# Performance work log

Measured on AMD Instinct MI355X. Metric: run time of the kernel, lower is better.

The kernel has to match this reference:

```python
import jax, jax.numpy as jnp
import numpy as np

N = 100000      # num vertices
NE = 20000      # num hyperedges
NNZ = 1600000   # incidence pairs
NFEAT = 128
NHID = 64       # nhid * nhead = 8 * 8
NCLASS = 40
NLAYER = 4
ALPHA = 0.1
LAMDA = 0.5


def setup_inputs() -> dict:
    key = jax.random.key(0)
    ks = jax.random.split(key, 9)
    x = jax.random.normal(ks[0], (N, NFEAT), dtype=jnp.float32)
    vertex = jax.random.randint(ks[1], (NNZ,), 0, N, dtype=jnp.int32)
    edges = jax.random.randint(ks[2], (NNZ,), 0, NE, dtype=jnp.int32)
    degE = jax.random.uniform(ks[3], (NE, 1), dtype=jnp.float32)
    degV = jax.random.uniform(ks[4], (N, 1), dtype=jnp.float32)
    W0 = jax.random.normal(ks[5], (NFEAT, NHID), dtype=jnp.float32) * 0.05
    b0 = jnp.zeros((NHID,), jnp.float32)
    Ws = jax.random.normal(ks[6], (NLAYER, NHID, NHID), dtype=jnp.float32) * 0.05
    Wout = jax.random.normal(ks[7], (NHID, NCLASS), dtype=jnp.float32) * 0.05
    bout = jnp.zeros((NCLASS,), jnp.float32)
    return dict(x=x, degE=degE, degV=degV, W0=W0, b0=b0, Ws=Ws,
                Wout=Wout, bout=bout, vertex=vertex, edges=edges)


def _normalize_l2(X):
    # torch: norm computed on detached X, inf scales zeroed
    norm = jnp.linalg.norm(jax.lax.stop_gradient(X), axis=1, keepdims=True)
    scale = jnp.where(norm > 0, 1.0 / norm, 0.0)
    return X * scale


def reference(x, degE, degV, W0, b0, Ws, Wout, bout, vertex, edges):
    # per-hyperedge member counts for the 'mean' first_aggregate
    counts = jax.ops.segment_sum(jnp.ones((NNZ,), x.dtype), edges, num_segments=NE)
    counts = jnp.maximum(counts, 1.0)[:, None]  # [NE,1]

    X = jax.nn.relu(x @ W0 + b0)   # [N, NHID]
    X0 = X
    for i in range(NLAYER):
        beta = float(np.log(LAMDA / (i + 1) + 1.0))
        Xve = X[vertex]                                                   # [NNZ, NHID]
        Xe = jax.ops.segment_sum(Xve, edges, num_segments=NE) / counts   # vertex->edge mean
        Xe = Xe * degE                                                    # [NE, NHID]
        Xev = Xe[edges]                                                   # [NNZ, NHID]
        Xv = jax.ops.segment_sum(Xev, vertex, num_segments=N) * degV     # edge->vertex sum
        Xn = _normalize_l2(Xv)                                            # use_norm=True
        Xi = (1.0 - ALPHA) * Xn + ALPHA * X0
        X = jax.nn.relu((1.0 - beta) * Xi + beta * (Xi @ Ws[i]))
    logits = X @ Wout + bout
    return jax.nn.log_softmax(logits, axis=1)
```

## Files before the change

kernel.cpp:

```cpp
#include <hip/hip_runtime.h>
#include <math.h>

constexpr int NV   = 100000;
constexpr int NEg  = 20000;
constexpr int NNZp = 1600000;
constexpr int NF   = 128;
constexpr int NH   = 64;
constexpr int NC   = 40;

constexpr int WE  = 64;
constexpr int NBE = (NEg + WE - 1) / WE;
constexpr int WV  = 256;
constexpr int NBV = (NV + WV - 1) / WV;
constexpr int CAPS = 6400;
constexpr int CH   = 4096;
constexpr int PBLK = (NNZp + CH - 1) / CH;

typedef __bf16 bf16x8 __attribute__((ext_vector_type(8)));
typedef float  f32x4  __attribute__((ext_vector_type(4)));
typedef unsigned short u16x8 __attribute__((ext_vector_type(8)));

__device__ __forceinline__ float bf2f(unsigned short u) {
    unsigned int x = ((unsigned int)u) << 16;
    return __builtin_bit_cast(float, x);
}
__device__ __forceinline__ unsigned short f2bf(float f) {
    unsigned int x = __builtin_bit_cast(unsigned int, f);
    x += 0x7fffu + ((x >> 16) & 1u);
    return (unsigned short)(x >> 16);
}
__device__ __forceinline__ ushort4 pack4(float a, float b, float c, float d) {
    ushort4 u; u.x = f2bf(a); u.y = f2bf(b); u.z = f2bf(c); u.w = f2bf(d);
    return u;
}

__device__ __forceinline__ int block_excl_scan(int val, int tid, int* wtot) {
    __syncthreads();
    int x = val;
#pragma unroll
    for (int o = 1; o < 64; o <<= 1) {
        int y = __shfl_up(x, o);
        if ((tid & 63) >= o) x += y;
    }
    if ((tid & 63) == 63) wtot[tid >> 6] = x;
    __syncthreads();
    int add = 0;
    const int w = tid >> 6;
#pragma unroll
    for (int k = 0; k < 7; ++k) add += (k < w) ? wtot[k] : 0;
    return add + x - val;
}

__global__ __launch_bounds__(256) void coarse_hist(const int* __restrict__ vertex,
                                                   const int* __restrict__ edges,
                                                   int* __restrict__ cnt_be,
                                                   int* __restrict__ cnt_bv) {
    __shared__ int he[NBE], hv[NBV];
    for (int i = threadIdx.x; i < NBE; i += 256) he[i] = 0;
    for (int i = threadIdx.x; i < NBV; i += 256) hv[i] = 0;
    __syncthreads();
    const int base = blockIdx.x * CH;
    const int end  = min(base + CH, NNZp);
    for (int i = base + threadIdx.x; i < end; i += 256) {
        atomicAdd(&he[edges[i]  >> 6], 1);
        atomicAdd(&hv[vertex[i] >> 8], 1);
    }
    __syncthreads();
    for (int i = threadIdx.x; i < NBE; i += 256) if (he[i]) atomicAdd(&cnt_be[i], he[i]);
    for (int i = threadIdx.x; i < NBV; i += 256) if (hv[i]) atomicAdd(&cnt_bv[i], hv[i]);
}

__global__ __launch_bounds__(512) void scan_buckets(const int* __restrict__ cnt_be,
                                                    const int* __restrict__ cnt_bv,
                                                    int* __restrict__ rsb_e,
                                                    int* __restrict__ rsb_v,
                                                    int* __restrict__ rs_e,
                                                    int* __restrict__ rs_v) {
    __shared__ int s[512];
    const int n      = (blockIdx.x == 0) ? NBE : NBV;
    const int* c     = (blockIdx.x == 0) ? cnt_be : cnt_bv;
    int* r           = (blockIdx.x == 0) ? rsb_e : rsb_v;
    const int t = threadIdx.x;
    int v = (t < n) ? c[t] : 0;
    s[t] = v;
    __syncthreads();
    for (int o = 1; o < 512; o <<= 1) {
        int u = (t >= o) ? s[t - o] : 0;
        __syncthreads();
        s[t] += u;
        __syncthreads();
    }
    if (t < n) r[t] = s[t] - v;
    if (t == 0) {
        r[n] = NNZp;
        if (blockIdx.x == 0) rs_e[NEg] = NNZp;
        else                 rs_v[NV]  = NNZp;
    }
}

__global__ __launch_bounds__(512) void partition_both(const int* __restrict__ vertex,
                                                      const int* __restrict__ edges,
                                                      const int* __restrict__ rsb_e,
                                                      const int* __restrict__ rsb_v,
                                                      int* __restrict__ gcur_e,
                                                      int* __restrict__ gcur_v,
                                                      int* __restrict__ vid_out,
                                                      int* __restrict__ eid_out) {
    __shared__ int sval_e[CH], sdst_e[CH];
    __shared__ int sval_v[CH], sdst_v[CH];
    __shared__ int hist_e[NBE], off_e[NBE], gbase_e[NBE], cnt_e[NBE];
    __shared__ int hist_v[NBV], off_v[NBV], gbase_v[NBV], cnt_v[NBV];
    __shared__ int wtot[8];
    const int tid = threadIdx.x;
    for (int i = tid; i < NBE; i += 512) { hist_e[i] = 0; cnt_e[i] = 0; }
    for (int i = tid; i < NBV; i += 512) { hist_v[i] = 0; cnt_v[i] = 0; }
    __syncthreads();
    const int base = blockIdx.x * CH;
    const int n    = min(base + CH, NNZp) - base;
    for (int i = tid; i < n; i += 512) {
        atomicAdd(&hist_e[edges[base + i]  >> 6], 1);
        atomicAdd(&hist_v[vertex[base + i] >> 8], 1);
    }
    __syncthreads();
    {
        int hv_ = (tid < NBE) ? hist_e[tid] : 0;
        int ex  = block_excl_scan(hv_, tid, wtot);
        if (tid < NBE) {
            off_e[tid]   = ex;
            gbase_e[tid] = rsb_e[tid] + (hv_ ? atomicAdd(&gcur_e[tid], hv_) : 0);
        }
    }
    {
        int hv_ = (tid < NBV) ? hist_v[tid] : 0;
        int ex  = block_excl_scan(hv_, tid, wtot);
        if (tid < NBV) {
            off_v[tid]   = ex;
            gbase_v[tid] = rsb_v[tid] + (hv_ ? atomicAdd(&gcur_v[tid], hv_) : 0);
        }
    }
    __syncthreads();
    for (int i = tid; i < n; i += 512) {
        int e = edges[base + i];
        int v = vertex[base + i];
        int fe = e >> 6;
        int rk = atomicAdd(&cnt_e[fe], 1);
        int sl = off_e[fe] + rk;
        sval_e[sl] = (v << 6) | (e & 63);
        sdst_e[sl] = gbase_e[fe] + rk;
        int fv = v >> 8;
        int rv = atomicAdd(&cnt_v[fv], 1);
        int s2 = off_v[fv] + rv;
        sval_v[s2] = (e << 8) | (v & 255);
        sdst_v[s2] = gbase_v[fv] + rv;
    }
    __syncthreads();
    for (int i = tid; i < n; i += 512) {
        vid_out[sdst_e[i]] = sval_e[i];
        eid_out[sdst_v[i]] = sval_v[i];
    }
}

__global__ __launch_bounds__(512) void local_sort_both(const int* __restrict__ rsb_e,
                                                       const int* __restrict__ rsb_v,
                                                       int* __restrict__ vid_buf,
                                                       int* __restrict__ eid_buf,
                                                       int* __restrict__ rs_e,
                                                       int* __restrict__ rs_v,
                                                       const float* __restrict__ degE,
                                                       float* __restrict__ scaleE) {
    __shared__ int stage[CAPS];
    __shared__ int hist[256], off[256], cnt2[256];
    const bool eside = blockIdx.x < NBE;
    const int b   = eside ? blockIdx.x : blockIdx.x - NBE;
    const int W   = eside ? 64 : 256;
    const int FB  = eside ? 6 : 8;
    const int NID = eside ? NEg : NV;
    const int* rsb = eside ? rsb_e : rsb_v;
    int* buf       = eside ? vid_buf : eid_buf;
    int* rs        = eside ? rs_e : rs_v;
    const int base = rsb[b];
    const int sz   = rsb[b + 1] - base;
    const int tid = threadIdx.x;
    if (tid < 256) { hist[tid] = 0; cnt2[tid] = 0; }
    __syncthreads();
    for (int t = tid; t < sz; t += 512) atomicAdd(&hist[buf[base + t] & (W - 1)], 1);
    __syncthreads();
    {
        int v = (tid < W) ? hist[tid] : 0;
        if (tid < W) off[tid] = v;
        __syncthreads();
        for (int o = 1; o < W; o <<= 1) {
            int u = (tid < W && tid >= o) ? off[tid - o] : 0;
            __syncthreads();
            if (tid < W) off[tid] += u;
            __syncthreads();
        }
        if (tid < W) off[tid] -= v;
    }
    if (tid < W) {
        int gid = b * W + tid;
        if (gid < NID) {
            rs[gid] = base + off[tid];
            if (eside) {
                int c = hist[tid];
                scaleE[gid] = degE[gid] / (float)(c < 1 ? 1 : c);
            }
        }
    }
    __syncthreads();
    for (int t = tid; t < sz; t += 512) {
        int w = buf[base + t];
        int f = w & (W - 1);
        int rk = off[f] + atomicAdd(&cnt2[f], 1);
        stage[rk] = w >> FB;
    }
    __syncthreads();
    for (int t = tid; t < sz; t += 512) buf[base + t] = stage[t];
}

__global__ __launch_bounds__(256) void make_wfrag(const float* __restrict__ Ws,
                                                  const float* __restrict__ Wout,
                                                  const float* __restrict__ W0,
                                                  unsigned short* __restrict__ frag) {
    int t = blockIdx.x * 256 + threadIdx.x;
    int lane = t & 63;
    int g = t >> 6;
    int quad = lane >> 4, cl = lane & 15;
    unsigned short o[8];
    if (g < 32) {
        int li = g >> 3, w = (g >> 1) & 3, kh = g & 1;
        int n = w * 16 + cl;
#pragma unroll
        for (int j = 0; j < 8; ++j) {
            int k = kh * 32 + quad * 8 + j;
            o[j] = f2bf(Ws[(size_t)li * NH * NH + k * NH + n]);
        }
    } else if (g < 40) {
        int w = (g - 32) >> 1, kh = g & 1;
        int n = w * 16 + cl;
#pragma unroll
        for (int j = 0; j < 8; ++j) {
            int k = kh * 32 + quad * 8 + j;
            o[j] = (n < NC) ? f2bf(Wout[k * NC + n]) : (unsigned short)0;
        }
    } else {
        int w = (g - 40) >> 2, kb = (g - 40) & 3;
        int n = w * 16 + cl;
#pragma unroll
        for (int j = 0; j < 8; ++j) {
            int k = kb * 32 + quad * 8 + j;
            o[j] = f2bf(W0[k * NH + n]);
        }
    }
    unsigned short* dst = frag + (size_t)g * 512 + lane * 8;
    *((ushort4*)dst)       = *(ushort4*)&o[0];
    *((ushort4*)(dst + 4)) = *(ushort4*)&o[4];
}

__global__ __launch_bounds__(256) void gemm0_kernel(const float* __restrict__ x,
                                                    const unsigned short* __restrict__ W0frag,
                                                    const float* __restrict__ b0,
                                                    unsigned short* __restrict__ Xbf,
                                                    unsigned short* __restrict__ X0bf) {
    __shared__ unsigned short xs[16][136];
    const int tid = threadIdx.x;
    const int r  = tid >> 4;
    const int c8 = (tid & 15) * 8;
    const int rowbase = blockIdx.x * 16;
    float4 p0 = *((const float4*)(x + (size_t)(rowbase + r) * NF + c8));
    float4 p1 = *((const float4*)(x + (size_t)(rowbase + r) * NF + c8 + 4));
    *((ushort4*)&xs[r][c8])     = pack4(p0.x, p0.y, p0.z, p0.w);
    *((ushort4*)&xs[r][c8 + 4]) = pack4(p1.x, p1.y, p1.z, p1.w);
    __syncthreads();
    const int lane = tid & 63;
    const int wv   = tid >> 6;
    const int quad = lane >> 4;
    const int cl   = lane & 15;
    f32x4 acc = {0.f, 0.f, 0.f, 0.f};
#pragma unroll
    for (int kb = 0; kb < 4; ++kb) {
        bf16x8 a = *((const bf16x8*)&xs[cl][kb * 32 + quad * 8]);
        bf16x8 b = *((const bf16x8*)(W0frag + ((size_t)(wv * 4 + kb) * 64 + lane) * 8));
        acc = __builtin_amdgcn_mfma_f32_16x16x32_bf16(a, b, acc, 0, 0, 0);
    }
    const int col = wv * 16 + cl;
    const float bo = b0[col];
#pragma unroll
    for (int p = 0; p < 4; ++p) {
        const int orow = quad * 4 + p;
        float o = acc[p] + bo;
        o = o > 0.f ? o : 0.f;
        unsigned short ob = f2bf(o);
        const size_t idx = (size_t)(rowbase + orow) * NH + col;
        Xbf[idx]  = ob;
        X0bf[idx] = ob;
    }
}

__global__ __launch_bounds__(256) void gather_ve(const int* __restrict__ rs_e,
                                                 const int* __restrict__ vid_sorted,
                                                 const unsigned short* __restrict__ Xbf,
                                                 const float* __restrict__ scaleE,
                                                 unsigned short* __restrict__ Xebf) {
    const int tid = threadIdx.x;
    const int l8  = tid & 7;
    const int e = blockIdx.x * 16 + (tid >> 4);
    const int sb = rs_e[e];
    const int se = rs_e[e + 1];
    const int h  = (se - sb + 1) >> 1;
    int m        = sb + ((tid & 8) ? h : 0);
    const int en = (tid & 8) ? se : (sb + h);
    float a[8] = {0.f, 0.f, 0.f, 0.f, 0.f, 0.f, 0.f, 0.f};
    if (m + 4 <= en) {
        int i0 = vid_sorted[m], i1 = vid_sorted[m + 1];
        int i2 = vid_sorted[m + 2], i3 = vid_sorted[m + 3];
        m += 4;
        while (m + 4 <= en) {
            int j0 = vid_sorted[m], j1 = vid_sorted[m + 1];
            int j2 = vid_sorted[m + 2], j3 = vid_sorted[m + 3];
            m += 4;
            u16x8 p = *((const u16x8*)(Xbf + (size_t)i0 * NH) + l8);
            u16x8 q = *((const u16x8*)(Xbf + (size_t)i1 * NH) + l8);
            u16x8 u = *((const u16x8*)(Xbf + (size_t)i2 * NH) + l8);
            u16x8 t = *((const u16x8*)(Xbf + (size_t)i3 * NH) + l8);
#pragma unroll
            for (int j = 0; j < 8; ++j)
                a[j] += bf2f(p[j]) + bf2f(q[j]) + bf2f(u[j]) + bf2f(t[j]);
            i0 = j0; i1 = j1; i2 = j2; i3 = j3;
        }
        u16x8 p = *((const u16x8*)(Xbf + (size_t)i0 * NH) + l8);
        u16x8 q = *((const u16x8*)(Xbf + (size_t)i1 * NH) + l8);
        u16x8 u = *((const u16x8*)(Xbf + (size_t)i2 * NH) + l8);
        u16x8 t = *((const u16x8*)(Xbf + (size_t)i3 * NH) + l8);
#pragma unroll
        for (int j = 0; j < 8; ++j)
            a[j] += bf2f(p[j]) + bf2f(q[j]) + bf2f(u[j]) + bf2f(t[j]);
    }
    for (; m < en; ++m) {
        u16x8 p = *((const u16x8*)(Xbf + (size_t)vid_sorted[m] * NH) + l8);
#pragma unroll
        for (int j = 0; j < 8; ++j) a[j] += bf2f(p[j]);
    }
#pragma unroll
    for (int j = 0; j < 8; ++j) a[j] += __shfl_xor(a[j], 8);
    if (!(tid & 8)) {
        const float s = scaleE[e];
        u16x8 o;
#pragma unroll
        for (int j = 0; j < 8; ++j) o[j] = f2bf(a[j] * s);
        *((u16x8*)(Xebf + (size_t)e * NH) + l8) = o;
    }
}

template <bool LAST>
__global__ __launch_bounds__(256) void gather_ev_update(const int* __restrict__ rs_v,
                                                        const int* __restrict__ eid_sorted,
                                                        const unsigned short* __restrict__ Xebf,
                                                        const float* __restrict__ degV,
                                                        const unsigned short* __restrict__ X0bf,
                                                        const unsigned short* __restrict__ WfragL,
                                                        unsigned short* __restrict__ Xbf,
                                                        float beta,
                                                        const unsigned short* __restrict__ WfragH,
                                                        const float* __restrict__ bout,
                                                        float* __restrict__ outp) {
    __shared__ unsigned short xis_bf[16][72];
    __shared__ unsigned short xo_bf[LAST ? 16 * 72 : 1];
    __shared__ float lg[LAST ? 16 * 48 : 1];
    const int tid = threadIdx.x;
    const int l8  = tid & 7;
    const int r   = tid >> 4;
    const int v = blockIdx.x * 16 + r;
    const int sb  = rs_v[v];
    const int sen = rs_v[v + 1];
    const float dv = degV[v];
    const int h  = (sen - sb + 1) >> 1;
    int m        = sb + ((tid & 8) ? h : 0);
    const int en = (tid & 8) ? sen : (sb + h);
    float a[8] = {0.f, 0.f, 0.f, 0.f, 0.f, 0.f, 0.f, 0.f};
    if (m + 4 <= en) {
        int i0 = eid_sorted[m], i1 = eid_sorted[m + 1];
        int i2 = eid_sorted[m + 2], i3 = eid_sorted[m + 3];
        m += 4;
        while (m + 4 <= en) {
            int j0 = eid_sorted[m], j1 = eid_sorted[m + 1];
            int j2 = eid_sorted[m + 2], j3 = eid_sorted[m + 3];
            m += 4;
            u16x8 p = *((const u16x8*)(Xebf + (size_t)i0 * NH) + l8);
            u16x8 q = *((const u16x8*)(Xebf + (size_t)i1 * NH) + l8);
            u16x8 u = *((const u16x8*)(Xebf + (size_t)i2 * NH) + l8);
            u16x8 t = *((const u16x8*)(Xebf + (size_t)i3 * NH) + l8);
#pragma unroll
            for (int j = 0; j < 8; ++j)
                a[j] += bf2f(p[j]) + bf2f(q[j]) + bf2f(u[j]) + bf2f(t[j]);
            i0 = j0; i1 = j1; i2 = j2; i3 = j3;
        }
        u16x8 p = *((const u16x8*)(Xebf + (size_t)i0 * NH) + l8);
        u16x8 q = *((const u16x8*)(Xebf + (size_t)i1 * NH) + l8);
        u16x8 u = *((const u16x8*)(Xebf + (size_t)i2 * NH) + l8);
        u16x8 t = *((const u16x8*)(Xebf + (size_t)i3 * NH) + l8);
#pragma unroll
        for (int j = 0; j < 8; ++j)
            a[j] += bf2f(p[j]) + bf2f(q[j]) + bf2f(u[j]) + bf2f(t[j]);
    }
    for (; m < en; ++m) {
        u16x8 p = *((const u16x8*)(Xebf + (size_t)eid_sorted[m] * NH) + l8);
#pragma unroll
        for (int j = 0; j < 8; ++j) a[j] += bf2f(p[j]);
    }
#pragma unroll
    for (int j = 0; j < 8; ++j) {
        a[j] += __shfl_xor(a[j], 8);
        a[j] *= dv;
    }
    float sq = 0.f;
#pragma unroll
    for (int j = 0; j < 8; ++j) sq += a[j] * a[j];
    sq += __shfl_xor(sq, 1);
    sq += __shfl_xor(sq, 2);
    sq += __shfl_xor(sq, 4);
    float norm = sqrtf(sq);
    float inv = norm > 0.f ? 1.f / norm : 0.f;
    u16x8 u0 = *((const u16x8*)(X0bf + (size_t)v * NH) + l8);
    if (!(tid & 8)) {
        u16x8 o;
#pragma unroll
        for (int j = 0; j < 8; ++j) o[j] = f2bf(0.9f * a[j] * inv + 0.1f * bf2f(u0[j]));
        *((u16x8*)&xis_bf[r][l8 * 8]) = o;
    }
    __syncthreads();

    const int lane = tid & 63;
    const int wv   = tid >> 6;
    const int quad = lane >> 4;
    const int cl   = lane & 15;
    bf16x8 bw0 = *((const bf16x8*)(WfragL + ((size_t)(wv * 2 + 0) * 64 + lane) * 8));
    bf16x8 bw1 = *((const bf16x8*)(WfragL + ((size_t)(wv * 2 + 1) * 64 + lane) * 8));
    bf16x8 a0 = *((const bf16x8*)&xis_bf[cl][quad * 8]);
    bf16x8 a1 = *((const bf16x8*)&xis_bf[cl][32 + quad * 8]);
    f32x4 acc = {0.f, 0.f, 0.f, 0.f};
    acc = __builtin_amdgcn_mfma_f32_16x16x32_bf16(a0, bw0, acc, 0, 0, 0);
    acc = __builtin_amdgcn_mfma_f32_16x16x32_bf16(a1, bw1, acc, 0, 0, 0);

    const float ob = 1.f - beta;
    const int col = wv * 16 + cl;
#pragma unroll
    for (int p = 0; p < 4; ++p) {
        const int row = quad * 4 + p;
        float xiv = bf2f(xis_bf[row][col]);
        float o = ob * xiv + beta * acc[p];
        o = o > 0.f ? o : 0.f;
        if (!LAST) {
            Xbf[(size_t)(blockIdx.x * 16 + row) * NH + col] = f2bf(o);
        } else {
            xo_bf[row * 72 + col] = f2bf(o);
        }
    }
    if (LAST) {
        __syncthreads();
        bf16x8 bh0 = *((const bf16x8*)(WfragH + ((size_t)(wv * 2 + 0) * 64 + lane) * 8));
        bf16x8 bh1 = *((const bf16x8*)(WfragH + ((size_t)(wv * 2 + 1) * 64 + lane) * 8));
        bf16x8 ah0 = *((const bf16x8*)&xo_bf[cl * 72 + quad * 8]);
        bf16x8 ah1 = *((const bf16x8*)&xo_bf[cl * 72 + 32 + quad * 8]);
        f32x4 acch = {0.f, 0.f, 0.f, 0.f};
        acch = __builtin_amdgcn_mfma_f32_16x16x32_bf16(ah0, bh0, acch, 0, 0, 0);
        acch = __builtin_amdgcn_mfma_f32_16x16x32_bf16(ah1, bh1, acch, 0, 0, 0);
        if (col < NC) {
            float bo = bout[col];
#pragma unroll
            for (int p = 0; p < 4; ++p) lg[(quad * 4 + p) * 48 + col] = acch[p] + bo;
        }
        __syncthreads();
        const int r0 = wv * 4;
        const bool act = lane < NC;
        float a0s = act ? lg[(r0 + 0) * 48 + lane] : -INFINITY;
        float a1s = act ? lg[(r0 + 1) * 48 + lane] : -INFINITY;
        float a2s = act ? lg[(r0 + 2) * 48 + lane] : -INFINITY;
        float a3s = act ? lg[(r0 + 3) * 48 + lane] : -INFINITY;
        float m0 = a0s, m1 = a1s, m2 = a2s, m3 = a3s;
#pragma unroll
        for (int o = 32; o; o >>= 1) {
            m0 = fmaxf(m0, __shfl_xor(m0, o));
            m1 = fmaxf(m1, __shfl_xor(m1, o));
            m2 = fmaxf(m2, __shfl_xor(m2, o));
            m3 = fmaxf(m3, __shfl_xor(m3, o));
        }
        float e0 = act ? expf(a0s - m0) : 0.f;
        float e1 = act ? expf(a1s - m1) : 0.f;
        float e2 = act ? expf(a2s - m2) : 0.f;
        float e3 = act ? expf(a3s - m3) : 0.f;
#pragma unroll
        for (int o = 32; o; o >>= 1) {
            e0 += __shfl_xor(e0, o);
            e1 += __shfl_xor(e1, o);
            e2 += __shfl_xor(e2, o);
            e3 += __shfl_xor(e3, o);
        }
        if (act) {
            const size_t vb = (size_t)(blockIdx.x * 16 + r0) * NC + lane;
            outp[vb + 0 * NC] = a0s - m0 - logf(e0);
            outp[vb + 1 * NC] = a1s - m1 - logf(e1);
            outp[vb + 2 * NC] = a2s - m2 - logf(e2);
            outp[vb + 3 * NC] = a3s - m3 - logf(e3);
        }
    }
}

extern "C" void kernel_launch(void* const* d_in, const int* in_sizes, int n_in,
                              void* d_out, int out_size, void* d_ws, size_t ws_size,
                              hipStream_t stream) {
    const float* x    = (const float*)d_in[0];
    const float* degE = (const float*)d_in[1];
    const float* degV = (const float*)d_in[2];
    const float* W0   = (const float*)d_in[3];
    const float* b0   = (const float*)d_in[4];
    const float* Ws   = (const float*)d_in[5];
    const float* Wout = (const float*)d_in[6];
    const float* bout = (const float*)d_in[7];
    const int* vertex = (const int*)d_in[8];
    const int* edges  = (const int*)d_in[9];
    float* out = (float*)d_out;

    float* scaleE = (float*)d_ws;
    unsigned short* Xbf  = (unsigned short*)(scaleE + NEg);
    unsigned short* X0bf = Xbf + (size_t)NV * NH;
    unsigned short* Xebf = X0bf + (size_t)NV * NH;
    int* cnt_be = (int*)(Xebf + (size_t)NEg * NH);
    int* cnt_bv = cnt_be + NBE;
    int* gcur_e = cnt_bv + NBV;
    int* gcur_v = gcur_e + NBE;
    int* rsb_e  = gcur_v + NBV;
    int* rsb_v  = rsb_e + (NBE + 1);
    int* rs_e   = rsb_v + (NBV + 1);
    int* rs_v   = rs_e + (NEg + 1);
    int* vid_sorted = rs_v + (NV + 1);
    int* eid_sorted = vid_sorted + NNZp;
    unsigned short* Wfrag = (unsigned short*)(eid_sorted + NNZp);

    hipMemsetAsync(cnt_be, 0, (size_t)(NBE + NBV) * 2 * sizeof(int), stream);
    make_wfrag<<<14, 256, 0, stream>>>(Ws, Wout, W0, Wfrag);
    coarse_hist<<<PBLK, 256, 0, stream>>>(vertex, edges, cnt_be, cnt_bv);
    scan_buckets<<<2, 512, 0, stream>>>(cnt_be, cnt_bv, rsb_e, rsb_v, rs_e, rs_v);
    partition_both<<<PBLK, 512, 0, stream>>>(vertex, edges, rsb_e, rsb_v,
                                             gcur_e, gcur_v, vid_sorted, eid_sorted);
    local_sort_both<<<NBE + NBV, 512, 0, stream>>>(rsb_e, rsb_v, vid_sorted, eid_sorted,
                                                   rs_e, rs_v, degE, scaleE);

    gemm0_kernel<<<NV / 16, 256, 0, stream>>>(x, Wfrag + 40 * 512, b0, Xbf, X0bf);

    const float betas[4] = {logf(0.5f / 1.f + 1.f), logf(0.5f / 2.f + 1.f),
                            logf(0.5f / 3.f + 1.f), logf(0.5f / 4.f + 1.f)};

    for (int i = 0; i < 3; ++i) {
        gather_ve<<<NEg / 16, 256, 0, stream>>>(rs_e, vid_sorted, Xbf, scaleE, Xebf);
        gather_ev_update<false><<<NV / 16, 256, 0, stream>>>(rs_v, eid_sorted, Xebf, degV,
                                                             X0bf, Wfrag + (size_t)i * 4096,
                                                             Xbf, betas[i],
                                                             nullptr, nullptr, nullptr);
    }
    gather_ve<<<NEg / 16, 256, 0, stream>>>(rs_e, vid_sorted, Xbf, scaleE, Xebf);
    gather_ev_update<true><<<NV / 16, 256, 0, stream>>>(rs_v, eid_sorted, Xebf, degV,
                                                        X0bf, Wfrag + (size_t)3 * 4096,
                                                        Xbf, betas[3],
                                                        Wfrag + 16384, bout, out);
}
```

Measured before the change: 391.1 us.

## Store per-block bucket histograms with column scan; deepen gather prefetch pipelines

New measurement: 425.2 us. 1.09x slower.

```diff
diff --git a/kernel.cpp b/kernel.cpp
--- a/kernel.cpp
+++ b/kernel.cpp
@@ -12,6 +12,7 @@
 constexpr int NBE = (NEg + WE - 1) / WE;
 constexpr int WV  = 256;
 constexpr int NBV = (NV + WV - 1) / WV;
+constexpr int SB  = NBE + NBV;
 constexpr int CAPS = 6400;
 constexpr int CH   = 4096;
 constexpr int PBLK = (NNZp + CH - 1) / CH;
@@ -33,6 +34,10 @@
     ushort4 u; u.x = f2bf(a); u.y = f2bf(b); u.z = f2bf(c); u.w = f2bf(d);
     return u;
 }
+__device__ __forceinline__ void acc8(float* a, u16x8 p) {
+#pragma unroll
+    for (int k = 0; k < 8; ++k) a[k] += bf2f(p[k]);
+}
 
 __device__ __forceinline__ int block_excl_scan(int val, int tid, int* wtot) {
     __syncthreads();
@@ -54,7 +59,8 @@
 __global__ __launch_bounds__(256) void coarse_hist(const int* __restrict__ vertex,
                                                    const int* __restrict__ edges,
                                                    int* __restrict__ cnt_be,
-                                                   int* __restrict__ cnt_bv) {
+                                                   int* __restrict__ cnt_bv,
+                                                   int* __restrict__ bhist) {
     __shared__ int he[NBE], hv[NBV];
     for (int i = threadIdx.x; i < NBE; i += 256) he[i] = 0;
     for (int i = threadIdx.x; i < NBV; i += 256) hv[i] = 0;
@@ -66,8 +72,17 @@
         atomicAdd(&hv[vertex[i] >> 8], 1);
     }
     __syncthreads();
-    for (int i = threadIdx.x; i < NBE; i += 256) if (he[i]) atomicAdd(&cnt_be[i], he[i]);
-    for (int i = threadIdx.x; i < NBV; i += 256) if (hv[i]) atomicAdd(&cnt_bv[i], hv[i]);
+    int* row = bhist + (size_t)blockIdx.x * SB;
+    for (int i = threadIdx.x; i < NBE; i += 256) {
+        int h = he[i];
+        row[i] = h;
+        if (h) atomicAdd(&cnt_be[i], h);
+    }
+    for (int i = threadIdx.x; i < NBV; i += 256) {
+        int h = hv[i];
+        row[NBE + i] = h;
+        if (h) atomicAdd(&cnt_bv[i], h);
+    }
 }
 
 __global__ __launch_bounds__(512) void scan_buckets(const int* __restrict__ cnt_be,
@@ -98,47 +113,56 @@
     }
 }
 
+__global__ __launch_bounds__(512) void colscan(const int* __restrict__ bhist,
+                                               const int* __restrict__ rsb_e,
+                                               const int* __restrict__ rsb_v,
+                                               int* __restrict__ abase) {
+    __shared__ int s[512];
+    const int f = blockIdx.x;
+    const int t = threadIdx.x;
+    int v = (t < PBLK) ? bhist[(size_t)t * SB + f] : 0;
+    s[t] = v;
+    __syncthreads();
+    for (int o = 1; o < 512; o <<= 1) {
+        int u = (t >= o) ? s[t - o] : 0;
+        __syncthreads();
+        s[t] += u;
+        __syncthreads();
+    }
+    const int base = (f < NBE) ? rsb_e[f] : rsb_v[f - NBE];
+    if (t < PBLK) abase[(size_t)t * SB + f] = base + (s[t] - v);
+}
+
 __global__ __launch_bounds__(512) void partition_both(const int* __restrict__ vertex,
                                                       const int* __restrict__ edges,
-                                                      const int* __restrict__ rsb_e,
-                                                      const int* __restrict__ rsb_v,
-                                                      int* __restrict__ gcur_e,
-                                                      int* __restrict__ gcur_v,
+                                                      const int* __restrict__ bhist,
+                                                      const int* __restrict__ abase,
                                                       int* __restrict__ vid_out,
                                                       int* __restrict__ eid_out) {
     __shared__ int sval_e[CH], sdst_e[CH];
     __shared__ int sval_v[CH], sdst_v[CH];
-    __shared__ int hist_e[NBE], off_e[NBE], gbase_e[NBE], cnt_e[NBE];
-    __shared__ int hist_v[NBV], off_v[NBV], gbase_v[NBV], cnt_v[NBV];
+    __shared__ int off_e[NBE], gb_e[NBE], cnt_e[NBE];
+    __shared__ int off_v[NBV], gb_v[NBV], cnt_v[NBV];
     __shared__ int wtot[8];
     const int tid = threadIdx.x;
-    for (int i = tid; i < NBE; i += 512) { hist_e[i] = 0; cnt_e[i] = 0; }
-    for (int i = tid; i < NBV; i += 512) { hist_v[i] = 0; cnt_v[i] = 0; }
-    __syncthreads();
-    const int base = blockIdx.x * CH;
+    const int b = blockIdx.x;
+    const int* bh = bhist + (size_t)b * SB;
+    const int* ab = abase + (size_t)b * SB;
+    for (int i = tid; i < NBE; i += 512) { cnt_e[i] = 0; gb_e[i] = ab[i]; }
+    for (int i = tid; i < NBV; i += 512) { cnt_v[i] = 0; gb_v[i] = ab[NBE + i]; }
+    {
+        int h  = (tid < NBE) ? bh[tid] : 0;
+        int ex = block_excl_scan(h, tid, wtot);
+        if (tid < NBE) off_e[tid] = ex;
+    }
+    {
+        int h  = (tid < NBV) ? bh[NBE + tid] : 0;
+        int ex = block_excl_scan(h, tid, wtot);
+        if (tid < NBV) off_v[tid] = ex;
+    }
+    __syncthreads();
+    const int base = b * CH;
     const int n    = min(base + CH, NNZp) - base;
-    for (int i = tid; i < n; i += 512) {
-        atomicAdd(&hist_e[edges[base + i]  >> 6], 1);
-        atomicAdd(&hist_v[vertex[base + i] >> 8], 1);
-    }
-    __syncthreads();
-    {
-        int hv_ = (tid < NBE) ? hist_e[tid] : 0;
-        int ex  = block_excl_scan(hv_, tid, wtot);
-        if (tid < NBE) {
-            off_e[tid]   = ex;
-            gbase_e[tid] = rsb_e[tid] + (hv_ ? atomicAdd(&gcur_e[tid], hv_) : 0);
-        }
-    }
-    {
-        int hv_ = (tid < NBV) ? hist_v[tid] : 0;
-        int ex  = block_excl_scan(hv_, tid, wtot);
-        if (tid < NBV) {
-            off_v[tid]   = ex;
-            gbase_v[tid] = rsb_v[tid] + (hv_ ? atomicAdd(&gcur_v[tid], hv_) : 0);
-        }
-    }
-    __syncthreads();
     for (int i = tid; i < n; i += 512) {
         int e = edges[base + i];
         int v = vertex[base + i];
@@ -146,12 +170,12 @@
         int rk = atomicAdd(&cnt_e[fe], 1);
         int sl = off_e[fe] + rk;
         sval_e[sl] = (v << 6) | (e & 63);
-        sdst_e[sl] = gbase_e[fe] + rk;
+        sdst_e[sl] = gb_e[fe] + rk;
         int fv = v >> 8;
         int rv = atomicAdd(&cnt_v[fv], 1);
         int s2 = off_v[fv] + rv;
         sval_v[s2] = (e << 8) | (v & 255);
-        sdst_v[s2] = gbase_v[fv] + rv;
+        sdst_v[s2] = gb_v[fv] + rv;
     }
     __syncthreads();
     for (int i = tid; i < n; i += 512) {
@@ -311,35 +335,59 @@
     int m        = sb + ((tid & 8) ? h : 0);
     const int en = (tid & 8) ? se : (sb + h);
     float a[8] = {0.f, 0.f, 0.f, 0.f, 0.f, 0.f, 0.f, 0.f};
-    if (m + 4 <= en) {
-        int i0 = vid_sorted[m], i1 = vid_sorted[m + 1];
-        int i2 = vid_sorted[m + 2], i3 = vid_sorted[m + 3];
-        m += 4;
-        while (m + 4 <= en) {
-            int j0 = vid_sorted[m], j1 = vid_sorted[m + 1];
-            int j2 = vid_sorted[m + 2], j3 = vid_sorted[m + 3];
-            m += 4;
-            u16x8 p = *((const u16x8*)(Xbf + (size_t)i0 * NH) + l8);
-            u16x8 q = *((const u16x8*)(Xbf + (size_t)i1 * NH) + l8);
-            u16x8 u = *((const u16x8*)(Xbf + (size_t)i2 * NH) + l8);
-            u16x8 t = *((const u16x8*)(Xbf + (size_t)i3 * NH) + l8);
+    const int nfull = (en - m) >> 3;
+    if (nfull >= 2) {
+        int idB[8];
+        u16x8 dA[8];
+        {
+            int idA[8];
+#pragma unroll
+            for (int j = 0; j < 8; ++j) idA[j] = vid_sorted[m + j];
 #pragma unroll
             for (int j = 0; j < 8; ++j)
-                a[j] += bf2f(p[j]) + bf2f(q[j]) + bf2f(u[j]) + bf2f(t[j]);
-            i0 = j0; i1 = j1; i2 = j2; i3 = j3;
-        }
-        u16x8 p = *((const u16x8*)(Xbf + (size_t)i0 * NH) + l8);
-        u16x8 q = *((const u16x8*)(Xbf + (size_t)i1 * NH) + l8);
-        u16x8 u = *((const u16x8*)(Xbf + (size_t)i2 * NH) + l8);
-        u16x8 t = *((const u16x8*)(Xbf + (size_t)i3 * NH) + l8);
+                dA[j] = *((const u16x8*)(Xbf + (size_t)idA[j] * NH) + l8);
+        }
+#pragma unroll
+        for (int j = 0; j < 8; ++j) idB[j] = vid_sorted[m + 8 + j];
+        m += 16;
+        for (int c = 2; c < nfull; ++c) {
+            u16x8 dB[8];
+#pragma unroll
+            for (int j = 0; j < 8; ++j)
+                dB[j] = *((const u16x8*)(Xbf + (size_t)idB[j] * NH) + l8);
+#pragma unroll
+            for (int j = 0; j < 8; ++j) idB[j] = vid_sorted[m + j];
+            m += 8;
+#pragma unroll
+            for (int j = 0; j < 8; ++j) acc8(a, dA[j]);
+#pragma unroll
+            for (int j = 0; j < 8; ++j) dA[j] = dB[j];
+        }
+        {
+            u16x8 dB[8];
+#pragma unroll
+            for (int j = 0; j < 8; ++j)
+                dB[j] = *((const u16x8*)(Xbf + (size_t)idB[j] * NH) + l8);
+#pragma unroll
+            for (int j = 0; j < 8; ++j) acc8(a, dA[j]);
+#pragma unroll
+            for (int j = 0; j < 8; ++j) acc8(a, dB[j]);
+        }
+    } else if (nfull == 1) {
+        int id[8];
+        u16x8 d[8];
+#pragma unroll
+        for (int j = 0; j < 8; ++j) id[j] = vid_sorted[m + j];
 #pragma unroll
         for (int j = 0; j < 8; ++j)
-            a[j] += bf2f(p[j]) + bf2f(q[j]) + bf2f(u[j]) + bf2f(t[j]);
+            d[j] = *((const u16x8*)(Xbf + (size_t)id[j] * NH) + l8);
+        m += 8;
+#pragma unroll
+        for (int j = 0; j < 8; ++j) acc8(a, d[j]);
     }
     for (; m < en; ++m) {
         u16x8 p = *((const u16x8*)(Xbf + (size_t)vid_sorted[m] * NH) + l8);
-#pragma unroll
-        for (int j = 0; j < 8; ++j) a[j] += bf2f(p[j]);
+        acc8(a, p);
     }
 #pragma unroll
     for (int j = 0; j < 8; ++j) a[j] += __shfl_xor(a[j], 8);
@@ -378,35 +426,59 @@
     int m        = sb + ((tid & 8) ? h : 0);
     const int en = (tid & 8) ? sen : (sb + h);
     float a[8] = {0.f, 0.f, 0.f, 0.f, 0.f, 0.f, 0.f, 0.f};
-    if (m + 4 <= en) {
-        int i0 = eid_sorted[m], i1 = eid_sorted[m + 1];
-        int i2 = eid_sorted[m + 2], i3 = eid_sorted[m + 3];
+    const int nfull = (en - m) >> 2;
+    if (nfull >= 2) {
+        int idB[4];
+        u16x8 dA[4];
+        {
+            int idA[4];
+#pragma unroll
+            for (int j = 0; j < 4; ++j) idA[j] = eid_sorted[m + j];
+#pragma unroll
+            for (int j = 0; j < 4; ++j)
+                dA[j] = *((const u16x8*)(Xebf + (size_t)idA[j] * NH) + l8);
+        }
+#pragma unroll
+        for (int j = 0; j < 4; ++j) idB[j] = eid_sorted[m + 4 + j];
+        m += 8;
+        for (int c = 2; c < nfull; ++c) {
+            u16x8 dB[4];
+#pragma unroll
+            for (int j = 0; j < 4; ++j)
+                dB[j] = *((const u16x8*)(Xebf + (size_t)idB[j] * NH) + l8);
+#pragma unroll
+            for (int j = 0; j < 4; ++j) idB[j] = eid_sorted[m + j];
+            m += 4;
+#pragma unroll
+            for (int j = 0; j < 4; ++j) acc8(a, dA[j]);
+#pragma unroll
+            for (int j = 0; j < 4; ++j) dA[j] = dB[j];
+        }
+        {
+            u16x8 dB[4];
+#pragma unroll
+            for (int j = 0; j < 4; ++j)
+                dB[j] = *((const u16x8*)(Xebf + (size_t)idB[j] * NH) + l8);
+#pragma unroll
+            for (int j = 0; j < 4; ++j) acc8(a, dA[j]);
+#pragma unroll
+            for (int j = 0; j < 4; ++j) acc8(a, dB[j]);
+        }
+    } else if (nfull == 1) {
+        int id[4];
+        u16x8 d[4];
+#pragma unroll
+        for (int j = 0; j < 4; ++j) id[j] = eid_sorted[m + j];
+#pragma unroll
+        for (int j = 0; j < 4; ++j)
+            d[j] = *((const u16x8*)(Xebf + (size_t)id[j] * NH) + l8);
         m += 4;
-        while (m + 4 <= en) {
-            int j0 = eid_sorted[m], j1 = eid_sorted[m + 1];
-            int j2 = eid_sorted[m + 2], j3 = eid_sorted[m + 3];
-            m += 4;
-            u16x8 p = *((const u16x8*)(Xebf + (size_t)i0 * NH) + l8);
-            u16x8 q = *((const u16x8*)(Xebf + (size_t)i1 * NH) + l8);
-            u16x8 u = *((const u16x8*)(Xebf + (size_t)i2 * NH) + l8);
-            u16x8 t = *((const u16x8*)(Xebf + (size_t)i3 * NH) + l8);
-#pragma unroll
-            for (int j = 0; j < 8; ++j)
-                a[j] += bf2f(p[j]) + bf2f(q[j]) + bf2f(u[j]) + bf2f(t[j]);
-            i0 = j0; i1 = j1; i2 = j2; i3 = j3;
-        }
-        u16x8 p = *((const u16x8*)(Xebf + (size_t)i0 * NH) + l8);
-        u16x8 q = *((const u16x8*)(Xebf + (size_t)i1 * NH) + l8);
-        u16x8 u = *((const u16x8*)(Xebf + (size_t)i2 * NH) + l8);
-        u16x8 t = *((const u16x8*)(Xebf + (size_t)i3 * NH) + l8);
-#pragma unroll
-        for (int j = 0; j < 8; ++j)
-            a[j] += bf2f(p[j]) + bf2f(q[j]) + bf2f(u[j]) + bf2f(t[j]);
+#pragma unroll
+        for (int j = 0; j < 4; ++j) acc8(a, d[j]);
     }
     for (; m < en; ++m) {
         u16x8 p = *((const u16x8*)(Xebf + (size_t)eid_sorted[m] * NH) + l8);
-#pragma unroll
-        for (int j = 0; j < 8; ++j) a[j] += bf2f(p[j]);
+        acc8(a, p);
     }
 #pragma unroll
     for (int j = 0; j < 8; ++j) {
@@ -527,22 +599,23 @@
     unsigned short* Xebf = X0bf + (size_t)NV * NH;
     int* cnt_be = (int*)(Xebf + (size_t)NEg * NH);
     int* cnt_bv = cnt_be + NBE;
-    int* gcur_e = cnt_bv + NBV;
-    int* gcur_v = gcur_e + NBE;
-    int* rsb_e  = gcur_v + NBV;
+    int* rsb_e  = cnt_bv + NBV;
     int* rsb_v  = rsb_e + (NBE + 1);
     int* rs_e   = rsb_v + (NBV + 1);
     int* rs_v   = rs_e + (NEg + 1);
     int* vid_sorted = rs_v + (NV + 1);
     int* eid_sorted = vid_sorted + NNZp;
     unsigned short* Wfrag = (unsigned short*)(eid_sorted + NNZp);
-
-    hipMemsetAsync(cnt_be, 0, (size_t)(NBE + NBV) * 2 * sizeof(int), stream);
+    int* bhist = (int*)(Wfrag + 56 * 512);
+    int* abase = bhist + (size_t)PBLK * SB;
+
+    hipMemsetAsync(cnt_be, 0, (size_t)(NBE + NBV) * sizeof(int), stream);
     make_wfrag<<<14, 256, 0, stream>>>(Ws, Wout, W0, Wfrag);
-    coarse_hist<<<PBLK, 256, 0, stream>>>(vertex, edges, cnt_be, cnt_bv);
+    coarse_hist<<<PBLK, 256, 0, stream>>>(vertex, edges, cnt_be, cnt_bv, bhist);
     scan_buckets<<<2, 512, 0, stream>>>(cnt_be, cnt_bv, rsb_e, rsb_v, rs_e, rs_v);
-    partition_both<<<PBLK, 512, 0, stream>>>(vertex, edges, rsb_e, rsb_v,
-                                             gcur_e, gcur_v, vid_sorted, eid_sorted);
+    colscan<<<SB, 512, 0, stream>>>(bhist, rsb_e, rsb_v, abase);
+    partition_both<<<PBLK, 512, 0, stream>>>(vertex, edges, bhist, abase,
+                                             vid_sorted, eid_sorted);
     local_sort_both<<<NBE + NBV, 512, 0, stream>>>(rsb_e, rsb_v, vid_sorted, eid_sorted,
                                                    rs_e, rs_v, degE, scaleE);
 
```
